# Optimization experiments

Hardware: AMD Instinct MI355X
Metric: run time of the kernel (lower is better)

The kernel has to match this reference:

```python
import jax, jax.numpy as jnp
import numpy as np


def setup_inputs() -> dict:
    key = jax.random.key(0)
    ks = jax.random.split(key, 6)
    B, V, C, T = 32, 2048, 64, 64
    x = jax.random.normal(ks[0], (B, V, C, T), dtype=jnp.float32)
    U_1 = jax.random.normal(ks[1], (V,), dtype=jnp.float32)
    U_2 = jax.random.normal(ks[2], (C, V), dtype=jnp.float32)
    U_3 = jax.random.normal(ks[3], (C,), dtype=jnp.float32)
    b_e = jax.random.normal(ks[4], (1, T, T), dtype=jnp.float32)
    V_e = jax.random.normal(ks[5], (B, T, T), dtype=jnp.float32)
    return {"x": x, "U_1": U_1, "U_2": U_2, "U_3": U_3, "b_e": b_e, "V_e": V_e}


def reference(x, U_1, U_2, U_3, b_e, V_e):
    # x: (B, V, C, T)
    # lhs = (x^T . U_1) . U_2  -> (B, T, V)
    lhs = jnp.einsum('bvct,v->btc', x, U_1) @ U_2          # (B,T,C) @ (C,V) -> (B,T,V)
    # rhs = x^T . U_3 -> (B, V, T)
    rhs = jnp.einsum('bvct,c->bvt', x, U_3)                # (B,V,T)
    product = jnp.einsum('btv,bvu->btu', lhs, rhs)          # (B,T,T)
    # E = V_e @ sigmoid(product + b_e); V_e broadcast over batch
    E = jnp.einsum('bts,bsu->btu', V_e, jax.nn.sigmoid(product + b_e))  # (B,T,T)
    # manual softmax along dim 1 (shift-invariant -> equivalent to jax.nn.softmax)
    return jax.nn.softmax(E, axis=1)
```

## Files before the change

kernel.cpp:

```cpp
#include <hip/hip_runtime.h>
#include <math.h>

#define NB 32
#define NV 2048
#define NC 64
#define NT 64
#define VC 64
#define CHUNKS (NV / VC)
#define U2P 68

__global__ __launch_bounds__(256) void k1_pass_x(
    const float* __restrict__ x,
    const float* __restrict__ U1,
    const float* __restrict__ U2,
    const float* __restrict__ U3,
    float* __restrict__ part)
{
    const int tid = threadIdx.x;
    const int blk = blockIdx.x;
    const int b     = blk / CHUNKS;
    const int chunk = blk % CHUNKS;
    const int v0    = chunk * VC;

    const int w    = tid >> 6;
    const int l    = tid & 63;
    const int u0   = (l & 15) * 4;
    const int crow = l >> 4;
    const int cw   = w * 16 + crow;

    __shared__ float U2s[VC][U2P];
    __shared__ float Msum[NC * NT];

    for (int i = tid; i < VC * NC; i += 256) {
        const int c  = i >> 6;
        const int vi = i & 63;
        U2s[vi][c] = U2[c * NV + v0 + vi];
    }

    float u3r[4];
#pragma unroll
    for (int k = 0; k < 4; ++k) u3r[k] = U3[cw + 4 * k];

    float4 t1r[4], mr[16];
#pragma unroll
    for (int k = 0; k < 4; ++k) t1r[k] = make_float4(0.f, 0.f, 0.f, 0.f);
#pragma unroll
    for (int j = 0; j < 16; ++j) mr[j] = make_float4(0.f, 0.f, 0.f, 0.f);

    __syncthreads();

    const float* xb = x + (size_t)(b * NV + v0) * (NC * NT) + cw * NT + u0;

    for (int vi = 0; vi < VC; ++vi) {
        const float* xv = xb + (size_t)vi * (NC * NT);

        float4 xa[4];
#pragma unroll
        for (int k = 0; k < 4; ++k)
            xa[k] = *reinterpret_cast<const float4*>(xv + 4 * k * NT);

        const float u1v = U1[v0 + vi];

        float4 rh = make_float4(0.f, 0.f, 0.f, 0.f);
#pragma unroll
        for (int k = 0; k < 4; ++k) {
            t1r[k].x = fmaf(u1v, xa[k].x, t1r[k].x);
            t1r[k].y = fmaf(u1v, xa[k].y, t1r[k].y);
            t1r[k].z = fmaf(u1v, xa[k].z, t1r[k].z);
            t1r[k].w = fmaf(u1v, xa[k].w, t1r[k].w);
            rh.x = fmaf(u3r[k], xa[k].x, rh.x);
            rh.y = fmaf(u3r[k], xa[k].y, rh.y);
            rh.z = fmaf(u3r[k], xa[k].z, rh.z);
            rh.w = fmaf(u3r[k], xa[k].w, rh.w);
        }

#pragma unroll
        for (int m = 16; m <= 32; m <<= 1) {
            rh.x += __shfl_xor(rh.x, m, 64);
            rh.y += __shfl_xor(rh.y, m, 64);
            rh.z += __shfl_xor(rh.z, m, 64);
            rh.w += __shfl_xor(rh.w, m, 64);
        }

#pragma unroll
        for (int j4 = 0; j4 < 4; ++j4) {
            const float4 u2v = *reinterpret_cast<const float4*>(
                &U2s[vi][crow * 16 + 4 * j4]);
            mr[4 * j4 + 0].x = fmaf(u2v.x, rh.x, mr[4 * j4 + 0].x);
            mr[4 * j4 + 0].y = fmaf(u2v.x, rh.y, mr[4 * j4 + 0].y);
            mr[4 * j4 + 0].z = fmaf(u2v.x, rh.z, mr[4 * j4 + 0].z);
            mr[4 * j4 + 0].w = fmaf(u2v.x, rh.w, mr[4 * j4 + 0].w);
            mr[4 * j4 + 1].x = fmaf(u2v.y, rh.x, mr[4 * j4 + 1].x);
            mr[4 * j4 + 1].y = fmaf(u2v.y, rh.y, mr[4 * j4 + 1].y);
            mr[4 * j4 + 1].z = fmaf(u2v.y, rh.z, mr[4 * j4 + 1].z);
            mr[4 * j4 + 1].w = fmaf(u2v.y, rh.w, mr[4 * j4 + 1].w);
            mr[4 * j4 + 2].x = fmaf(u2v.z, rh.x, mr[4 * j4 + 2].x);
            mr[4 * j4 + 2].y = fmaf(u2v.z, rh.y, mr[4 * j4 + 2].y);
            mr[4 * j4 + 2].z = fmaf(u2v.z, rh.z, mr[4 * j4 + 2].z);
            mr[4 * j4 + 2].w = fmaf(u2v.z, rh.w, mr[4 * j4 + 2].w);
            mr[4 * j4 + 3].x = fmaf(u2v.w, rh.x, mr[4 * j4 + 3].x);
            mr[4 * j4 + 3].y = fmaf(u2v.w, rh.y, mr[4 * j4 + 3].y);
            mr[4 * j4 + 3].z = fmaf(u2v.w, rh.z, mr[4 * j4 + 3].z);
            mr[4 * j4 + 3].w = fmaf(u2v.w, rh.w, mr[4 * j4 + 3].w);
        }
    }

    float* pb = part + (size_t)(b * CHUNKS + chunk) * 2 * NC * NT;

#pragma unroll
    for (int k = 0; k < 4; ++k)
        *reinterpret_cast<float4*>(&pb[(cw + 4 * k) * NT + u0]) = t1r[k];

    for (int i = 0; i < 4; ++i) {
        if (w == i) {
#pragma unroll
            for (int j = 0; j < 16; ++j) {
                float* d = &Msum[(crow * 16 + j) * NT + u0];
                if (i == 0) {
                    *reinterpret_cast<float4*>(d) = mr[j];
                } else {
                    d[0] += mr[j].x; d[1] += mr[j].y;
                    d[2] += mr[j].z; d[3] += mr[j].w;
                }
            }
        }
        __syncthreads();
    }

    float* pbM = pb + NC * NT;
    for (int i = tid * 4; i < NC * NT; i += 1024)
        *reinterpret_cast<float4*>(&pbM[i]) =
            *reinterpret_cast<const float4*>(&Msum[i]);
}

__global__ __launch_bounds__(256) void k2a_reduce(
    const float4* __restrict__ part4,
    float4* __restrict__ fin4)
{
    const int j = blockIdx.x;
    const int b = j >> 3;
    const int local = (j & 7) * 256 + threadIdx.x;

    const float4* p = part4 + (size_t)b * CHUNKS * 2048 + local;
    float4 a0 = make_float4(0.f, 0.f, 0.f, 0.f);
    float4 a1 = a0, a2 = a0, a3 = a0;
#pragma unroll
    for (int ch = 0; ch < CHUNKS; ch += 4) {
        const float4 v0 = p[(size_t)(ch + 0) * 2048];
        const float4 v1 = p[(size_t)(ch + 1) * 2048];
        const float4 v2 = p[(size_t)(ch + 2) * 2048];
        const float4 v3 = p[(size_t)(ch + 3) * 2048];
        a0.x += v0.x; a0.y += v0.y; a0.z += v0.z; a0.w += v0.w;
        a1.x += v1.x; a1.y += v1.y; a1.z += v1.z; a1.w += v1.w;
        a2.x += v2.x; a2.y += v2.y; a2.z += v2.z; a2.w += v2.w;
        a3.x += v3.x; a3.y += v3.y; a3.z += v3.z; a3.w += v3.w;
    }
    float4 acc;
    acc.x = (a0.x + a1.x) + (a2.x + a3.x);
    acc.y = (a0.y + a1.y) + (a2.y + a3.y);
    acc.z = (a0.z + a1.z) + (a2.z + a3.z);
    acc.w = (a0.w + a1.w) + (a2.w + a3.w);
    fin4[(size_t)b * 2048 + local] = acc;
}

__global__ __launch_bounds__(256) void k2b_epilogue(
    const float* __restrict__ fin,
    const float* __restrict__ b_e,
    const float* __restrict__ V_e,
    float* __restrict__ out)
{
    const int b = blockIdx.x;
    const int tid = threadIdx.x;

    __shared__ float t1[NC * NT];
    __shared__ float Mb[NC * NT];
    __shared__ float P[NT * NT];
    __shared__ float Eb[NT * NT];

    const float* t1g = fin + (size_t)b * 2 * NC * NT;
    const float* mgb = t1g + NC * NT;
    for (int i = tid * 4; i < NC * NT; i += 1024) {
        *reinterpret_cast<float4*>(&t1[i]) = *reinterpret_cast<const float4*>(&t1g[i]);
        *reinterpret_cast<float4*>(&Mb[i]) = *reinterpret_cast<const float4*>(&mgb[i]);
    }
    __syncthreads();

    const int u  = tid & 63;
    const int tg = tid >> 6;

    for (int i = 0; i < 16; ++i) {
        const int t = tg * 16 + i;
        float acc = 0.f;
#pragma unroll 8
        for (int c = 0; c < NC; ++c)
            acc = fmaf(t1[c * NT + t], Mb[c * NT + u], acc);
        const float z = acc + b_e[t * NT + u];
        P[t * NT + u] = 1.0f / (1.0f + expf(-z));
    }
    __syncthreads();

    const float* veb = V_e + (size_t)b * NT * NT;
    for (int i = 0; i < 16; ++i) {
        const int t = tg * 16 + i;
        float acc = 0.f;
#pragma unroll 8
        for (int s = 0; s < NT; ++s)
            acc = fmaf(veb[t * NT + s], P[s * NT + u], acc);
        Eb[t * NT + u] = acc;
    }
    __syncthreads();

    if (tid < NT) {
        const int uu = tid;
        float m = -INFINITY;
        for (int t = 0; t < NT; ++t) m = fmaxf(m, Eb[t * NT + uu]);
        float ssum = 0.f;
        for (int t = 0; t < NT; ++t) {
            const float e = expf(Eb[t * NT + uu] - m);
            Eb[t * NT + uu] = e;
            ssum += e;
        }
        const float inv = 1.0f / ssum;
        for (int t = 0; t < NT; ++t)
            out[(size_t)b * NT * NT + t * NT + uu] = Eb[t * NT + uu] * inv;
    }
}

extern "C" void kernel_launch(void* const* d_in, const int* in_sizes, int n_in,
                              void* d_out, int out_size, void* d_ws, size_t ws_size,
                              hipStream_t stream) {
    const float* x   = (const float*)d_in[0];
    const float* U1  = (const float*)d_in[1];
    const float* U2  = (const float*)d_in[2];
    const float* U3  = (const float*)d_in[3];
    const float* b_e = (const float*)d_in[4];
    const float* V_e = (const float*)d_in[5];
    float* out = (float*)d_out;

    float* part = (float*)d_ws;
    float* fin  = part + (size_t)NB * CHUNKS * 2 * NC * NT;

    k1_pass_x<<<NB * CHUNKS, 256, 0, stream>>>(x, U1, U2, U3, part);
    k2a_reduce<<<256, 256, 0, stream>>>((const float4*)part, (float4*)fin);
    k2b_epilogue<<<NB, 256, 0, stream>>>(fin, b_e, V_e, out);
}
```

Baseline: 257.2 us.

## Double-buffer x loads in registers and double the V-chunk per block

The main pass now prefetches the next pair of V slices of x into a second register buffer while computing on the current pair. This is meant to hide global-load latency in what is a bandwidth-bound stream over x. The chunk size grows from 64 to 128 V rows, which halves the number of blocks and the partial sums the reduce kernel has to read. A launch-bounds occupancy hint of 3 blocks per CU is added. The larger chunk doubles the U2 shared-memory tile and leaves only about two blocks per CU, which could reduce latency hiding. The extra register buffers may also cause spills.

```diff
diff --git a/kernel.cpp b/kernel.cpp
--- a/kernel.cpp
+++ b/kernel.cpp
@@ -5,11 +5,13 @@
 #define NV 2048
 #define NC 64
 #define NT 64
-#define VC 64
+#define VC 128
 #define CHUNKS (NV / VC)
 #define U2P 68
 
-__global__ __launch_bounds__(256) void k1_pass_x(
+typedef float f32x4 __attribute__((ext_vector_type(4)));
+
+__global__ __launch_bounds__(256, 3) void k1_pass_x(
     const float* __restrict__ x,
     const float* __restrict__ U1,
     const float* __restrict__ U2,
@@ -32,8 +34,8 @@
     __shared__ float Msum[NC * NT];
 
     for (int i = tid; i < VC * NC; i += 256) {
-        const int c  = i >> 6;
-        const int vi = i & 63;
+        const int c  = i >> 7;
+        const int vi = i & 127;
         U2s[vi][c] = U2[c * NV + v0 + vi];
     }
 
@@ -49,61 +51,86 @@
 
     __syncthreads();
 
-    const float* xb = x + (size_t)(b * NV + v0) * (NC * NT) + cw * NT + u0;
-
-    for (int vi = 0; vi < VC; ++vi) {
-        const float* xv = xb + (size_t)vi * (NC * NT);
-
-        float4 xa[4];
-#pragma unroll
-        for (int k = 0; k < 4; ++k)
-            xa[k] = *reinterpret_cast<const float4*>(xv + 4 * k * NT);
-
-        const float u1v = U1[v0 + vi];
-
-        float4 rh = make_float4(0.f, 0.f, 0.f, 0.f);
-#pragma unroll
-        for (int k = 0; k < 4; ++k) {
-            t1r[k].x = fmaf(u1v, xa[k].x, t1r[k].x);
-            t1r[k].y = fmaf(u1v, xa[k].y, t1r[k].y);
-            t1r[k].z = fmaf(u1v, xa[k].z, t1r[k].z);
-            t1r[k].w = fmaf(u1v, xa[k].w, t1r[k].w);
-            rh.x = fmaf(u3r[k], xa[k].x, rh.x);
-            rh.y = fmaf(u3r[k], xa[k].y, rh.y);
-            rh.z = fmaf(u3r[k], xa[k].z, rh.z);
-            rh.w = fmaf(u3r[k], xa[k].w, rh.w);
-        }
-
-#pragma unroll
-        for (int m = 16; m <= 32; m <<= 1) {
-            rh.x += __shfl_xor(rh.x, m, 64);
-            rh.y += __shfl_xor(rh.y, m, 64);
-            rh.z += __shfl_xor(rh.z, m, 64);
-            rh.w += __shfl_xor(rh.w, m, 64);
-        }
-
-#pragma unroll
-        for (int j4 = 0; j4 < 4; ++j4) {
-            const float4 u2v = *reinterpret_cast<const float4*>(
-                &U2s[vi][crow * 16 + 4 * j4]);
-            mr[4 * j4 + 0].x = fmaf(u2v.x, rh.x, mr[4 * j4 + 0].x);
-            mr[4 * j4 + 0].y = fmaf(u2v.x, rh.y, mr[4 * j4 + 0].y);
-            mr[4 * j4 + 0].z = fmaf(u2v.x, rh.z, mr[4 * j4 + 0].z);
-            mr[4 * j4 + 0].w = fmaf(u2v.x, rh.w, mr[4 * j4 + 0].w);
-            mr[4 * j4 + 1].x = fmaf(u2v.y, rh.x, mr[4 * j4 + 1].x);
-            mr[4 * j4 + 1].y = fmaf(u2v.y, rh.y, mr[4 * j4 + 1].y);
-            mr[4 * j4 + 1].z = fmaf(u2v.y, rh.z, mr[4 * j4 + 1].z);
-            mr[4 * j4 + 1].w = fmaf(u2v.y, rh.w, mr[4 * j4 + 1].w);
-            mr[4 * j4 + 2].x = fmaf(u2v.z, rh.x, mr[4 * j4 + 2].x);
-            mr[4 * j4 + 2].y = fmaf(u2v.z, rh.y, mr[4 * j4 + 2].y);
-            mr[4 * j4 + 2].z = fmaf(u2v.z, rh.z, mr[4 * j4 + 2].z);
-            mr[4 * j4 + 2].w = fmaf(u2v.z, rh.w, mr[4 * j4 + 2].w);
-            mr[4 * j4 + 3].x = fmaf(u2v.w, rh.x, mr[4 * j4 + 3].x);
-            mr[4 * j4 + 3].y = fmaf(u2v.w, rh.y, mr[4 * j4 + 3].y);
-            mr[4 * j4 + 3].z = fmaf(u2v.w, rh.z, mr[4 * j4 + 3].z);
-            mr[4 * j4 + 3].w = fmaf(u2v.w, rh.w, mr[4 * j4 + 3].w);
-        }
-    }
+    const float*  xb   = x + (size_t)(b * NV + v0) * (NC * NT) + cw * NT + u0;
+    const size_t  SLAB = (size_t)NC * NT;
+
+    f32x4 A[8], B[8];
+
+#define LOAD_PAIR(DST, PL)                                                 \
+    {                                                                      \
+        const float* xv_ = xb + (size_t)(PL) * 2 * SLAB;                   \
+        _Pragma("unroll")                                                  \
+        for (int s_ = 0; s_ < 2; ++s_) {                                   \
+            _Pragma("unroll")                                              \
+            for (int k_ = 0; k_ < 4; ++k_)                                 \
+                DST[s_ * 4 + k_] = *reinterpret_cast<const f32x4*>(        \
+                    xv_ + (size_t)s_ * SLAB + 4 * k_ * NT);                \
+        }                                                                  \
+    }
+
+#define COMPUTE_PAIR(SRC, PC)                                              \
+    {                                                                      \
+        _Pragma("unroll")                                                  \
+        for (int s_ = 0; s_ < 2; ++s_) {                                   \
+            const int   vv_  = 2 * (PC) + s_;                              \
+            const float u1v_ = U1[v0 + vv_];                               \
+            float4 rh_ = make_float4(0.f, 0.f, 0.f, 0.f);                  \
+            _Pragma("unroll")                                              \
+            for (int k_ = 0; k_ < 4; ++k_) {                               \
+                const f32x4 xa_ = SRC[s_ * 4 + k_];                        \
+                t1r[k_].x = fmaf(u1v_, xa_.x, t1r[k_].x);                  \
+                t1r[k_].y = fmaf(u1v_, xa_.y, t1r[k_].y);                  \
+                t1r[k_].z = fmaf(u1v_, xa_.z, t1r[k_].z);                  \
+                t1r[k_].w = fmaf(u1v_, xa_.w, t1r[k_].w);                  \
+                rh_.x = fmaf(u3r[k_], xa_.x, rh_.x);                       \
+                rh_.y = fmaf(u3r[k_], xa_.y, rh_.y);                       \
+                rh_.z = fmaf(u3r[k_], xa_.z, rh_.z);                       \
+                rh_.w = fmaf(u3r[k_], xa_.w, rh_.w);                       \
+            }                                                              \
+            _Pragma("unroll")                                              \
+            for (int m_ = 16; m_ <= 32; m_ <<= 1) {                        \
+                rh_.x += __shfl_xor(rh_.x, m_, 64);                        \
+                rh_.y += __shfl_xor(rh_.y, m_, 64);                        \
+                rh_.z += __shfl_xor(rh_.z, m_, 64);                        \
+                rh_.w += __shfl_xor(rh_.w, m_, 64);                        \
+            }                                                              \
+            _Pragma("unroll")                                              \
+            for (int j4_ = 0; j4_ < 4; ++j4_) {                            \
+                const float4 u2v_ = *reinterpret_cast<const float4*>(      \
+                    &U2s[vv_][crow * 16 + 4 * j4_]);                       \
+                mr[4 * j4_ + 0].x = fmaf(u2v_.x, rh_.x, mr[4 * j4_ + 0].x);\
+                mr[4 * j4_ + 0].y = fmaf(u2v_.x, rh_.y, mr[4 * j4_ + 0].y);\
+                mr[4 * j4_ + 0].z = fmaf(u2v_.x, rh_.z, mr[4 * j4_ + 0].z);\
+                mr[4 * j4_ + 0].w = fmaf(u2v_.x, rh_.w, mr[4 * j4_ + 0].w);\
+                mr[4 * j4_ + 1].x = fmaf(u2v_.y, rh_.x, mr[4 * j4_ + 1].x);\
+                mr[4 * j4_ + 1].y = fmaf(u2v_.y, rh_.y, mr[4 * j4_ + 1].y);\
+                mr[4 * j4_ + 1].z = fmaf(u2v_.y, rh_.z, mr[4 * j4_ + 1].z);\
+                mr[4 * j4_ + 1].w = fmaf(u2v_.y, rh_.w, mr[4 * j4_ + 1].w);\
+                mr[4 * j4_ + 2].x = fmaf(u2v_.z, rh_.x, mr[4 * j4_ + 2].x);\
+                mr[4 * j4_ + 2].y = fmaf(u2v_.z, rh_.y, mr[4 * j4_ + 2].y);\
+                mr[4 * j4_ + 2].z = fmaf(u2v_.z, rh_.z, mr[4 * j4_ + 2].z);\
+                mr[4 * j4_ + 2].w = fmaf(u2v_.z, rh_.w, mr[4 * j4_ + 2].w);\
+                mr[4 * j4_ + 3].x = fmaf(u2v_.w, rh_.x, mr[4 * j4_ + 3].x);\
+                mr[4 * j4_ + 3].y = fmaf(u2v_.w, rh_.y, mr[4 * j4_ + 3].y);\
+                mr[4 * j4_ + 3].z = fmaf(u2v_.w, rh_.z, mr[4 * j4_ + 3].z);\
+                mr[4 * j4_ + 3].w = fmaf(u2v_.w, rh_.w, mr[4 * j4_ + 3].w);\
+            }                                                              \
+        }                                                                  \
+    }
+
+    LOAD_PAIR(A, 0)
+
+    for (int p = 0; p < VC / 2; p += 2) {
+        const int pl1 = (p + 1 < VC / 2) ? p + 1 : p;
+        LOAD_PAIR(B, pl1)
+        COMPUTE_PAIR(A, p)
+        const int pl2 = (p + 2 < VC / 2) ? p + 2 : VC / 2 - 1;
+        LOAD_PAIR(A, pl2)
+        COMPUTE_PAIR(B, p + 1)
+    }
+
+#undef LOAD_PAIR
+#undef COMPUTE_PAIR
 
     float* pb = part + (size_t)(b * CHUNKS + chunk) * 2 * NC * NT;
 
```

Measured after the change: 351.1 us. +36.5%, slower.
